# Optimization experiments

Measured on AMD Instinct MI355X. Metric: run time of the kernel, lower is better.

Reference implementation:

```python
import jax, jax.numpy as jnp
import numpy as np

VX, VY = 0.16, 0.16
X_OFF = VX / 2 + 0.0          # vx/2 + point_cloud_range[0]
Y_OFF = VY / 2 + (-39.68)     # vy/2 + point_cloud_range[1]
BN_EPS = 1e-3


def setup_inputs() -> dict:
    key = jax.random.key(0)
    P, N, C_IN, C_OUT = 40000, 32, 9, 64
    k1, k2, k3, k4, k5, k6 = jax.random.split(key, 6)
    voxels = jax.random.normal(k1, (P, N, 4), dtype=jnp.float32)
    # at least 1 real point per pillar (avoids div-by-zero, matches real data)
    voxel_num_points = jax.random.randint(k2, (P,), 1, N + 1, dtype=jnp.int32)
    # coords layout: [batch_idx, z, y, x]
    voxel_coords = jax.random.randint(k3, (P, 4), 0, 432, dtype=jnp.int32)
    W = jax.random.normal(k4, (C_OUT, C_IN), dtype=jnp.float32) * 0.1  # 1x1 conv kernel
    gamma = jnp.ones((C_OUT,), jnp.float32)
    beta = jnp.zeros((C_OUT,), jnp.float32)
    running_mean = jax.random.normal(k5, (C_OUT,), jnp.float32) * 0.01
    running_var = jax.random.uniform(k6, (C_OUT,), jnp.float32, minval=0.5, maxval=1.5)
    return {
        "voxels": voxels,
        "W": W,
        "gamma": gamma,
        "beta": beta,
        "running_mean": running_mean,
        "running_var": running_var,
        "voxel_num_points": voxel_num_points,
        "voxel_coords": voxel_coords,
    }


def reference(voxels, W, gamma, beta, running_mean, running_var,
              voxel_num_points, voxel_coords):
    P, N, _ = voxels.shape
    npts = voxel_num_points.astype(voxels.dtype)[:, None, None]          # [P,1,1]
    points_mean = voxels[:, :, :3].sum(axis=1, keepdims=True) / npts     # [P,1,3]
    f_cluster = voxels[:, :, :3] - points_mean                           # [P,N,3]

    cx = voxel_coords[:, 3].astype(voxels.dtype)[:, None] * VX + X_OFF   # [P,1]
    cy = voxel_coords[:, 2].astype(voxels.dtype)[:, None] * VY + Y_OFF
    x_c = voxels[:, :, 0] - cx                                           # [P,N]
    y_c = voxels[:, :, 1] - cy

    # NOTE: torch code mutates features[:,:,:2] in place via the f_center view,
    # so the first two feature channels are ALSO the centered coordinates.
    feats = jnp.concatenate(
        [x_c[..., None], y_c[..., None], voxels[:, :, 2:4],
         f_cluster, x_c[..., None], y_c[..., None]], axis=-1)            # [P,N,9]

    mask = (jnp.arange(N)[None, :] < voxel_num_points[:, None]).astype(voxels.dtype)
    feats = feats * mask[..., None]

    # PFNLayer: 1x1 conv (no bias) + BatchNorm (eval) + ReLU + max over points
    x = jnp.einsum('pnc,oc->pno', feats, W)                              # [P,N,64]
    scale = gamma / jnp.sqrt(running_var + BN_EPS)
    x = (x - running_mean) * scale + beta
    x = jax.nn.relu(x)
    return x.max(axis=1)                                                 # [P,64] pillar_features
```

## Files before the change

### kernel.cpp

```cpp
#include <hip/hip_runtime.h>
#include <cstdint>


__global__ __launch_bounds__(256) void pillar_vfe_kernel(
    const float2* __restrict__ voxels2,
    const float*  __restrict__ Wp,
    const float*  __restrict__ gamma_p,
    const float*  __restrict__ beta_p,
    const float*  __restrict__ rmean_p,
    const float*  __restrict__ rvar_p,
    const int*    __restrict__ npts_p,
    const int*    __restrict__ coords_p,
    float*        __restrict__ out,
    int P)
{
    __shared__ float2 sh[4 * 64];

    const int tid    = threadIdx.x;
    const int pblock = blockIdx.x * 4;

    {
        const int gidx = pblock * 64 + tid;
        if (gidx < P * 64) sh[tid] = voxels2[gidx];
    }
    __syncthreads();

    const int wave = tid >> 6;
    const int lane = tid & 63;
    const int p    = pblock + wave;
    if (p >= P) return;

    const int   npts = npts_p[p];
    const float fn   = (float)npts;
    const float cx   = (float)coords_p[p * 4 + 3] * 0.16f + 0.08f;
    const float cy   = (float)coords_p[p * 4 + 2] * 0.16f + (0.08f - 39.68f);

    const float2* shp = sh + wave * 64;
    float sx = 0.f, sy = 0.f, sz = 0.f;
    if (lane < 32) {
        const float2 a = shp[lane * 2];
        const float2 b = shp[lane * 2 + 1];
        sx = a.x; sy = a.y; sz = b.x;
    }
    #pragma unroll
    for (int m = 16; m >= 1; m >>= 1) {
        sx += __shfl_xor(sx, m, 64);
        sy += __shfl_xor(sy, m, 64);
        sz += __shfl_xor(sz, m, 64);
    }
    sx = __shfl(sx, 0, 64);
    sy = __shfl(sy, 0, 64);
    sz = __shfl(sz, 0, 64);
    const float mx = sx / fn, my = sy / fn, mz = sz / fn;

    const int o = lane;
    float w[9];
    #pragma unroll
    for (int c = 0; c < 9; ++c) w[c] = Wp[o * 9 + c];
    const float g     = gamma_p[o];
    const float b     = beta_p[o];
    const float mu    = rmean_p[o];
    const float var   = rvar_p[o];
    const float scale = g / sqrtf(var + 1e-3f);

    const float A0 = (w[0] + w[4] + w[7]) * scale;
    const float A1 = (w[1] + w[5] + w[8]) * scale;
    const float A2 = (w[2] + w[6]) * scale;
    const float A3 = w[3] * scale;
    const float C0 = b - mu * scale;
    const float C  = C0 - (cx * (w[0] + w[7]) + cy * (w[1] + w[8])
                           + mx * w[4] + my * w[5] + mz * w[6]) * scale;

    float vmax = (npts < 32) ? fmaxf(C0, 0.0f) : -3.4e38f;

    for (int n = 0; n < npts; ++n) {
        const float2 a  = shp[n * 2];
        const float2 bu = shp[n * 2 + 1];
        float acc = C;
        acc = fmaf(a.x,  A0, acc);
        acc = fmaf(a.y,  A1, acc);
        acc = fmaf(bu.x, A2, acc);
        acc = fmaf(bu.y, A3, acc);
        vmax = fmaxf(vmax, acc);
    }
    vmax = fmaxf(vmax, 0.0f) * 0.0f + fmaxf(vmax, 0.0f);
    vmax = fmaxf(vmax, 0.0f);

    out[p * 64 + o] = vmax;
}

extern "C" void kernel_launch(void* const* d_in, const int* in_sizes, int n_in,
                              void* d_out, int out_size, void* d_ws, size_t ws_size,
                              hipStream_t stream) {
    const float2* voxels = (const float2*)d_in[0];
    const float*  W      = (const float*)d_in[1];
    const float*  gamma_ = (const float*)d_in[2];
    const float*  beta_  = (const float*)d_in[3];
    const float*  rmean  = (const float*)d_in[4];
    const float*  rvar   = (const float*)d_in[5];
    const int*    npts   = (const int*)d_in[6];
    const int*    coords = (const int*)d_in[7];
    float*        out    = (float*)d_out;

    const int P = in_sizes[6];
    const int blocks = (P + 3) / 4;

    pillar_vfe_kernel<<<blocks, 256, 0, stream>>>(
        voxels, W, gamma_, beta_, rmean, rvar, npts, coords, out, P);
}
```

Baseline: 102.3 us.

## Precompute folded BN weights in setup kernel and vectorize voxel loads

Adds a one-block setup kernel that folds BatchNorm scale and shift into per-channel conv coefficients and writes them to workspace, so the main kernel reads ten floats per lane instead of recomputing weights with a sqrt and divide. Voxels are staged through shared memory as float4 (one per point), and the main loop uses one float4 LDS per point. The cluster-mean term is subtracted after the max, since it is constant across points, so the mean reduction no longer sits on the loop's critical path. This adds a second kernel launch and a dependence on the workspace buffer.

```diff
diff --git a/kernel.cpp b/kernel.cpp
--- a/kernel.cpp
+++ b/kernel.cpp
@@ -2,26 +2,48 @@
 #include <cstdint>
 
 
+__global__ __launch_bounds__(64) void pillar_setup_kernel(
+    const float* __restrict__ Wp,
+    const float* __restrict__ gamma_p,
+    const float* __restrict__ beta_p,
+    const float* __restrict__ rmean_p,
+    const float* __restrict__ rvar_p,
+    float*       __restrict__ params)
+{
+    const int o = threadIdx.x;
+    float w[9];
+    #pragma unroll
+    for (int c = 0; c < 9; ++c) w[c] = Wp[o * 9 + c];
+    const float s = gamma_p[o] / sqrtf(rvar_p[o] + 1e-3f);
+
+    params[0 * 64 + o] = (w[0] + w[4] + w[7]) * s;
+    params[1 * 64 + o] = (w[1] + w[5] + w[8]) * s;
+    params[2 * 64 + o] = (w[2] + w[6]) * s;
+    params[3 * 64 + o] = w[3] * s;
+    params[4 * 64 + o] = beta_p[o] - rmean_p[o] * s;
+    params[5 * 64 + o] = (w[0] + w[7]) * s;
+    params[6 * 64 + o] = (w[1] + w[8]) * s;
+    params[7 * 64 + o] = w[4] * s;
+    params[8 * 64 + o] = w[5] * s;
+    params[9 * 64 + o] = w[6] * s;
+}
+
 __global__ __launch_bounds__(256) void pillar_vfe_kernel(
-    const float2* __restrict__ voxels2,
-    const float*  __restrict__ Wp,
-    const float*  __restrict__ gamma_p,
-    const float*  __restrict__ beta_p,
-    const float*  __restrict__ rmean_p,
-    const float*  __restrict__ rvar_p,
+    const float4* __restrict__ voxels4,
+    const float*  __restrict__ params,
     const int*    __restrict__ npts_p,
     const int*    __restrict__ coords_p,
     float*        __restrict__ out,
     int P)
 {
-    __shared__ float2 sh[4 * 64];
+    __shared__ float4 sh[4 * 32];
 
     const int tid    = threadIdx.x;
     const int pblock = blockIdx.x * 4;
 
-    {
-        const int gidx = pblock * 64 + tid;
-        if (gidx < P * 64) sh[tid] = voxels2[gidx];
+    if (tid < 128) {
+        const int gidx = pblock * 32 + tid;
+        if (gidx < P * 32) sh[tid] = voxels4[gidx];
     }
     __syncthreads();
 
@@ -30,69 +52,59 @@
     const int p    = pblock + wave;
     if (p >= P) return;
 
+    const float A0   = params[0 * 64 + lane];
+    const float A1   = params[1 * 64 + lane];
+    const float A2   = params[2 * 64 + lane];
+    const float A3   = params[3 * 64 + lane];
+    const float C0   = params[4 * 64 + lane];
+    const float SW07 = params[5 * 64 + lane];
+    const float SW18 = params[6 * 64 + lane];
+    const float SW4  = params[7 * 64 + lane];
+    const float SW5  = params[8 * 64 + lane];
+    const float SW6  = params[9 * 64 + lane];
+
     const int   npts = npts_p[p];
     const float fn   = (float)npts;
     const float cx   = (float)coords_p[p * 4 + 3] * 0.16f + 0.08f;
     const float cy   = (float)coords_p[p * 4 + 2] * 0.16f + (0.08f - 39.68f);
 
-    const float2* shp = sh + wave * 64;
+    const float4* shp = sh + wave * 32;
+
     float sx = 0.f, sy = 0.f, sz = 0.f;
     if (lane < 32) {
-        const float2 a = shp[lane * 2];
-        const float2 b = shp[lane * 2 + 1];
-        sx = a.x; sy = a.y; sz = b.x;
+        const float4 v = shp[lane];
+        sx = v.x; sy = v.y; sz = v.z;
     }
     #pragma unroll
-    for (int m = 16; m >= 1; m >>= 1) {
+    for (int m = 32; m >= 1; m >>= 1) {
         sx += __shfl_xor(sx, m, 64);
         sy += __shfl_xor(sy, m, 64);
         sz += __shfl_xor(sz, m, 64);
     }
-    sx = __shfl(sx, 0, 64);
-    sy = __shfl(sy, 0, 64);
-    sz = __shfl(sz, 0, 64);
-    const float mx = sx / fn, my = sy / fn, mz = sz / fn;
 
-    const int o = lane;
-    float w[9];
-    #pragma unroll
-    for (int c = 0; c < 9; ++c) w[c] = Wp[o * 9 + c];
-    const float g     = gamma_p[o];
-    const float b     = beta_p[o];
-    const float mu    = rmean_p[o];
-    const float var   = rvar_p[o];
-    const float scale = g / sqrtf(var + 1e-3f);
-
-    const float A0 = (w[0] + w[4] + w[7]) * scale;
-    const float A1 = (w[1] + w[5] + w[8]) * scale;
-    const float A2 = (w[2] + w[6]) * scale;
-    const float A3 = w[3] * scale;
-    const float C0 = b - mu * scale;
-    const float C  = C0 - (cx * (w[0] + w[7]) + cy * (w[1] + w[8])
-                           + mx * w[4] + my * w[5] + mz * w[6]) * scale;
-
-    float vmax = (npts < 32) ? fmaxf(C0, 0.0f) : -3.4e38f;
-
+    const float C1 = C0 - cx * SW07 - cy * SW18;
+    float vmax = -3.4e38f;
     for (int n = 0; n < npts; ++n) {
-        const float2 a  = shp[n * 2];
-        const float2 bu = shp[n * 2 + 1];
-        float acc = C;
-        acc = fmaf(a.x,  A0, acc);
-        acc = fmaf(a.y,  A1, acc);
-        acc = fmaf(bu.x, A2, acc);
-        acc = fmaf(bu.y, A3, acc);
+        const float4 v = shp[n];
+        float acc = C1;
+        acc  = fmaf(v.x, A0, acc);
+        acc  = fmaf(v.y, A1, acc);
+        acc  = fmaf(v.z, A2, acc);
+        acc  = fmaf(v.w, A3, acc);
         vmax = fmaxf(vmax, acc);
     }
-    vmax = fmaxf(vmax, 0.0f) * 0.0f + fmaxf(vmax, 0.0f);
-    vmax = fmaxf(vmax, 0.0f);
 
-    out[p * 64 + o] = vmax;
+    const float inv_n    = 1.0f / fn;
+    const float meanterm = (sx * SW4 + sy * SW5 + sz * SW6) * inv_n;
+    vmax -= meanterm;
+    if (npts < 32) vmax = fmaxf(vmax, C0);
+    out[p * 64 + lane] = fmaxf(vmax, 0.0f);
 }
 
 extern "C" void kernel_launch(void* const* d_in, const int* in_sizes, int n_in,
                               void* d_out, int out_size, void* d_ws, size_t ws_size,
                               hipStream_t stream) {
-    const float2* voxels = (const float2*)d_in[0];
+    const float4* voxels = (const float4*)d_in[0];
     const float*  W      = (const float*)d_in[1];
     const float*  gamma_ = (const float*)d_in[2];
     const float*  beta_  = (const float*)d_in[3];
@@ -101,10 +113,12 @@
     const int*    npts   = (const int*)d_in[6];
     const int*    coords = (const int*)d_in[7];
     float*        out    = (float*)d_out;
+    float*        params = (float*)d_ws;
 
     const int P = in_sizes[6];
+
+    pillar_setup_kernel<<<1, 64, 0, stream>>>(W, gamma_, beta_, rmean, rvar, params);
+
     const int blocks = (P + 3) / 4;
-
-    pillar_vfe_kernel<<<blocks, 256, 0, stream>>>(
-        voxels, W, gamma_, beta_, rmean, rvar, npts, coords, out, P);
+    pillar_vfe_kernel<<<blocks, 256, 0, stream>>>(voxels, params, npts, coords, out, P);
 }
```

Result: no change. 100.5 us (-1.8%).
